# Kernel tuning notes

Measured on AMD Instinct MI355X. Metric: run time of the kernel, lower is better.

## Reference

```python
import jax, jax.numpy as jnp
import numpy as np

D = 16        # flow dimensionality (args.d)
M = 128       # hidden nodes per layer
L = 2         # num_hidden_layers
B = 256       # batch
NF = 2        # num_flows
NORM_C = 1.0  # get_normalizing_const for initialization='sqrt-(m)'
STD_H = 1.0 / np.sqrt(M)  # give_std('sqrt-(m)', M)
STD_A = 0.1   # std for last layer


def _lower_mask(out, inp, d):
    # block lower-triangular (incl. diagonal) mask over d x d blocks
    return jnp.kron(jnp.tril(jnp.ones((d, d), jnp.float32)), jnp.ones((out // d, inp // d), jnp.float32))


def _diag_blocks(W, d):
    # extract the d diagonal blocks of W -> (d, out_blk, in_blk)
    ob, ib = W.shape[0] // d, W.shape[1] // d
    idx = jnp.arange(d)
    return W.reshape(d, ob, d, ib)[idx, :, idx, :]


def _init_W(key, out, inp, d, std):
    # 'clamp-zero' init: positive diagonal blocks, gaussian strictly-lower blocks, zero above
    W = std * jax.random.normal(key, (out, inp), dtype=jnp.float32)
    lm = _lower_mask(out, inp, d)
    dm = jnp.kron(jnp.eye(d, dtype=jnp.float32), jnp.ones((out // d, inp // d), jnp.float32))
    W = W * lm
    return jnp.where(dm > 0, jnp.clip(jnp.abs(W), 1e-10, None), W)


def _flow(inp, Ws, bs, d, norm_c):
    b = inp.shape[0]
    out, grad = inp, None
    nlay = len(bs)
    log_c = jnp.log(jnp.asarray(norm_c, inp.dtype))
    for i in range(nlay):
        W = Ws[i]
        wm = W * _lower_mask(W.shape[0], W.shape[1], d)
        lg = jnp.log(_diag_blocks(W, d))            # (d, ob, ib)
        if grad is None:
            grad = jnp.broadcast_to(lg[None], (b,) + lg.shape)  # (B, d, ob, 1)
        else:
            # log-space matvec over previous width: (B,d,ob,1)
            grad = jax.nn.logsumexp(lg[None, :, :, :, None] + grad[:, :, None, :, :], axis=3)
        out = out @ wm.T + bs[i]                    # (B, ob*d)
        # log |tanh'(out)| = 2*(log2 - out - softplus(-2 out))
        lga = 2.0 * (jnp.log(2.0) - out - jax.nn.softplus(-2.0 * out))
        out = norm_c * jnp.tanh(out)
        ob = W.shape[0] // d
        grad = grad + lga.reshape(b, d, ob, 1) + log_c
    # final (linear) layer
    W = Ws[nlay]
    wm = W * _lower_mask(W.shape[0], W.shape[1], d)
    lg = jnp.log(_diag_blocks(W, d))                # (d, 1, ib)
    grad = jax.nn.logsumexp(lg[None, :, :, :, None] + grad[:, :, None, :, :], axis=3)  # (B,d,1,1)
    out = out @ wm.T                                # (B, d)
    return out, grad.reshape(b, d).sum(-1)          # log-det Jacobian per sample


def setup_inputs() -> dict:
    key = jax.random.key(0)
    ks = jax.random.split(key, 11)
    inp = jax.random.normal(ks[0], (B, D), dtype=jnp.float32)
    params = {}
    for f in range(NF):
        o = 1 + 5 * f
        params[f'f{f}_W0'] = _init_W(ks[o + 0], M * D, D, D, STD_H)
        params[f'f{f}_W1'] = _init_W(ks[o + 1], M * D, M * D, D, STD_H)
        params[f'f{f}_W2'] = _init_W(ks[o + 2], D, M * D, D, STD_A)
        params[f'f{f}_b0'] = STD_H * jax.random.normal(ks[o + 3], (M * D,), dtype=jnp.float32)
        params[f'f{f}_b1'] = STD_H * jax.random.normal(ks[o + 4], (M * D,), dtype=jnp.float32)
    return {'inp': inp, **params}


def reference(inp, f0_W0, f0_W1, f0_W2, f0_b0, f0_b1, f1_W0, f1_W1, f1_W2, f1_b0, f1_b1):
    out, ld0 = _flow(inp, [f0_W0, f0_W1, f0_W2], [f0_b0, f0_b1], D, NORM_C)
    out, ld1 = _flow(out, [f1_W0, f1_W1, f1_W2], [f1_b0, f1_b1], D, NORM_C)
    return out, ld0 + ld1
```

## Files before the change

### kernel.cpp

```cpp
#include <hip/hip_runtime.h>
#include <stdint.h>

#define BATCH 256
#define DBLK  16
#define OB    128
#define NN    2048

using bf16x8  = __attribute__((ext_vector_type(8))) __bf16;
using f32x4   = __attribute__((ext_vector_type(4))) float;
using ushort8 = __attribute__((ext_vector_type(8))) unsigned short;

__device__ __forceinline__ unsigned short f2bf(float f) {
    union { float f; uint32_t u; } v; v.f = f;
    uint32_t u = v.u;
    uint32_t r = (u + 0x7fffu + ((u >> 16) & 1u)) >> 16;
    return (unsigned short)r;
}

__device__ __forceinline__ float bf2f(unsigned short h) {
    union { uint32_t u; float f; } v; v.u = ((uint32_t)h) << 16;
    return v.f;
}

__device__ __forceinline__ void act_tanh_lga(float x, float& th, float& lga) {
    float ax = fabsf(x);
    float e  = __expf(-2.f * ax);
    float p  = 1.f + e;
    float t  = 1.f - __fdividef(2.f * e, p);
    th  = (x < 0.f) ? -t : t;
    lga = 2.f * (0.69314718055994531f - ax - __logf(p));
}

__device__ __forceinline__ ushort8 pack_bf8(float4 a, float4 b) {
    ushort8 u;
    u[0] = f2bf(a.x); u[1] = f2bf(a.y); u[2] = f2bf(a.z); u[3] = f2bf(a.w);
    u[4] = f2bf(b.x); u[5] = f2bf(b.y); u[6] = f2bf(b.z); u[7] = f2bf(b.w);
    return u;
}

__device__ __forceinline__ void conv4pairs(int cid, int tid,
                                           const float* __restrict__ Wsrc,
                                           unsigned short* __restrict__ Wdst) {
    float4 va[3][2];
    unsigned short* dp[3];
    bool act[3];
    #pragma unroll
    for (int i = 0; i < 3; ++i) {
        const int c = tid + i * 512;
        act[i] = (c < 1088);
        if (act[i]) {
            const int pi  = c / 272;
            const int rem = c - pi * 272;
            const int p   = cid * 4 + pi;
            const int kend0 = ((p >> 7) + 1) * OB;
            const int off = rem * 8;
            const int row = (off < kend0) ? p : (NN - 1 - p);
            const int k   = (off < kend0) ? off : (off - kend0);
            const float* sp = Wsrc + (size_t)row * NN + k;
            dp[i] = Wdst + (size_t)row * NN + k;
            va[i][0] = *(const float4*)(sp);
            va[i][1] = *(const float4*)(sp + 4);
        }
    }
    #pragma unroll
    for (int i = 0; i < 3; ++i)
        if (act[i]) *(ushort8*)dp[i] = pack_bf8(va[i][0], va[i][1]);
}

__device__ __forceinline__ void l0_block512(const float* __restrict__ xs,
                                            const float* __restrict__ W0,
                                            const float* __restrict__ b0,
                                            unsigned short* __restrict__ h0,
                                            unsigned short* __restrict__ e0,
                                            float* __restrict__ mmax,
                                            int b, int t) {
    const int dd = t >> 5;
    const int j0 = dd * OB + (t & 31) * 4;
    float g[4];
    unsigned short hv[4];
    float lm = -1e30f;
    #pragma unroll
    for (int q = 0; q < 4; ++q) {
        const int j = j0 + q;
        const float* wrow = W0 + (size_t)j * DBLK;
        float s = b0[j];
        #pragma unroll
        for (int c = 0; c < DBLK; c += 4) {
            float4 wv = *(const float4*)(wrow + c);
            s += wv.x * xs[c] + wv.y * xs[c + 1] + wv.z * xs[c + 2] + wv.w * xs[c + 3];
        }
        float th, lga;
        act_tanh_lga(s, th, lga);
        hv[q] = f2bf(th);
        g[q]  = __logf(wrow[dd]) + lga;
        lm = fmaxf(lm, g[q]);
    }
    #pragma unroll
    for (int off = 1; off < 32; off <<= 1) lm = fmaxf(lm, __shfl_xor(lm, off));
    ushort4 hh, ee;
    #pragma unroll
    for (int q = 0; q < 4; ++q) {
        ((unsigned short*)&hh)[q] = hv[q];
        ((unsigned short*)&ee)[q] = f2bf(__expf(g[q] - lm));
    }
    *(ushort4*)(h0 + (size_t)b * NN + j0) = hh;
    *(ushort4*)(e0 + (size_t)b * NN + j0) = ee;
    if ((t & 31) == 0) mmax[b * DBLK + dd] = lm;
}

__global__ void __launch_bounds__(512)
k_prep(const float* __restrict__ W1a,
       unsigned short* __restrict__ W1bf,
       const float* __restrict__ inp,
       const float* __restrict__ W00,
       const float* __restrict__ b00,
       unsigned short* __restrict__ h0,
       unsigned short* __restrict__ e0,
       float* __restrict__ mmax) {
    const int gb = blockIdx.x;
    const int t  = threadIdx.x;
    if (gb < 256) {
        conv4pairs(gb, t, W1a, W1bf);
    } else {
        const int b = gb - 256;
        l0_block512(inp + (size_t)b * DBLK, W00, b00, h0, e0, mmax, b, t);
    }
}

template<bool CONV>
__global__ void __launch_bounds__(512, 4)
k_l1(const unsigned short* __restrict__ h0,
     const unsigned short* __restrict__ W1b,
     const float* __restrict__ b1v,
     const unsigned short* __restrict__ e0,
     const float* __restrict__ mmax,
     unsigned short* __restrict__ h1,
     float* __restrict__ g1,
     const float* __restrict__ W1next,
     unsigned short* __restrict__ W1bfn) {
    const int tid = threadIdx.x;

    if (CONV && blockIdx.z == 4) {
        const int cid = (int)blockIdx.x * 16 + (int)blockIdx.y;
        conv4pairs(cid, tid, W1next, W1bfn);
        return;
    }

    const int dd    = blockIdx.x;
    const int bt    = blockIdx.y;
    const int ct    = blockIdx.z;
    const int w     = tid >> 6;
    const int lane  = tid & 63;
    const int brow0 = bt * 16;
    const int arow  = brow0 + (lane & 15);
    const int koff  = (lane >> 4) * 8;
    const int ncol  = lane & 15;
    const int col0  = dd * OB + ct * 32;

    f32x4 acc[2], acc2[2];
    #pragma unroll
    for (int nt = 0; nt < 2; ++nt) {
        acc[nt]  = (f32x4){0.f, 0.f, 0.f, 0.f};
        acc2[nt] = (f32x4){0.f, 0.f, 0.f, 0.f};
    }

    const unsigned short* Ab = h0 + (size_t)arow * NN + koff;
    const unsigned short* Bb[2];
    #pragma unroll
    for (int nt = 0; nt < 2; ++nt)
        Bb[nt] = W1b + (size_t)(col0 + nt * 16 + ncol) * NN + koff;

    bf16x8 ga  = {};
    bf16x8 gb0 = {};
    bf16x8 gb1 = {};
    if (w < 4) {
        const int k2 = dd * OB + w * 32;
        ga  = *(const bf16x8*)(e0 + (size_t)arow * NN + koff + k2);
        gb0 = *(const bf16x8*)(Bb[0] + k2);
        gb1 = *(const bf16x8*)(Bb[1] + k2);
    }

    const int nch = (dd + 1) * 4;
    #pragma unroll 4
    for (int c = w; c < nch; c += 8) {
        const int k = c * 32;
        bf16x8 a   = *(const bf16x8*)(Ab + k);
        bf16x8 b0v = *(const bf16x8*)(Bb[0] + k);
        bf16x8 b1w = *(const bf16x8*)(Bb[1] + k);
        acc[0] = __builtin_amdgcn_mfma_f32_16x16x32_bf16(a, b0v, acc[0], 0, 0, 0);
        acc[1] = __builtin_amdgcn_mfma_f32_16x16x32_bf16(a, b1w, acc[1], 0, 0, 0);
    }

    if (w < 4) {
        acc2[0] = __builtin_amdgcn_mfma_f32_16x16x32_bf16(ga, gb0, acc2[0], 0, 0, 0);
        acc2[1] = __builtin_amdgcn_mfma_f32_16x16x32_bf16(ga, gb1, acc2[1], 0, 0, 0);
    }

    __shared__ float ls1[8][2][64][4];
    __shared__ float ls2[4][2][64][4];
    #pragma unroll
    for (int nt = 0; nt < 2; ++nt)
        *(f32x4*)&ls1[w][nt][lane][0] = acc[nt];
    if (w < 4) {
        #pragma unroll
        for (int nt = 0; nt < 2; ++nt)
            *(f32x4*)&ls2[w][nt][lane][0] = acc2[nt];
    }
    __syncthreads();

    {
        const int o  = tid;
        const int rr = o >> 5;
        const int cc = o & 31;
        const int nt = cc >> 4;
        const int r  = rr & 3;
        const int ls = (rr >> 2) * 16 + (cc & 15);
        float S = 0.f, S2 = 0.f;
        #pragma unroll
        for (int ww = 0; ww < 8; ++ww) S += ls1[ww][nt][ls][r];
        #pragma unroll
        for (int ww = 0; ww < 4; ++ww) S2 += ls2[ww][nt][ls][r];
        const int j    = col0 + cc;
        const int brow = brow0 + rr;
        const float pre = S + b1v[j];
        float th, lga;
        act_tanh_lga(pre, th, lga);
        h1[(size_t)brow * NN + j] = f2bf(th);
        g1[(size_t)brow * NN + j] = __logf(S2) + mmax[brow * DBLK + dd] + lga;
    }
}

__device__ __forceinline__ float final_compute(const unsigned short* __restrict__ h1,
                                               const float* __restrict__ g1,
                                               const float* __restrict__ W2,
                                               int b, int t,
                                               float* sh, float* gf, float* sx) {
    const int wave = t >> 6;
    const int lane = t & 63;
    {
        const int k = t * 4;
        ushort4 hv = *(const ushort4*)(h1 + (size_t)b * NN + k);
        float4 f0;
        f0.x = bf2f(hv.x); f0.y = bf2f(hv.y); f0.z = bf2f(hv.z); f0.w = bf2f(hv.w);
        *(float4*)(sh + k) = f0;
    }
    __syncthreads();

    #pragma unroll
    for (int q = 0; q < 2; ++q) {
        const int dd = wave + q * 8;
        const float* w2r = W2 + (size_t)dd * NN;
        const int kend = (dd + 1) * OB;
        float s = 0.f;
        for (int k = lane * 4; k < kend; k += 64 * 4) {
            float4 hv = *(const float4*)(sh + k);
            float4 wv = *(const float4*)(w2r + k);
            s += hv.x * wv.x + hv.y * wv.y + hv.z * wv.z + hv.w * wv.w;
        }
        #pragma unroll
        for (int off = 32; off > 0; off >>= 1) s += __shfl_xor(s, off);
        float v0 = g1[(size_t)b * NN + dd * OB + lane];
        float v1 = g1[(size_t)b * NN + dd * OB + 64 + lane];
        float m = fmaxf(v0, v1);
        #pragma unroll
        for (int off = 32; off > 0; off >>= 1) m = fmaxf(m, __shfl_xor(m, off));
        float e = __expf(v0 - m) * w2r[dd * OB + lane]
                + __expf(v1 - m) * w2r[dd * OB + 64 + lane];
        #pragma unroll
        for (int off = 32; off > 0; off >>= 1) e += __shfl_xor(e, off);
        if (lane == 0) {
            sx[dd] = s;
            gf[dd] = __logf(e) + m;
        }
    }
    __syncthreads();
    float ld = 0.f;
    #pragma unroll
    for (int dd = 0; dd < DBLK; ++dd) ld += gf[dd];
    return ld;
}

__global__ void __launch_bounds__(512)
k_fin0(const unsigned short* __restrict__ h1,
       const float* __restrict__ g1,
       const float* __restrict__ W2,
       const float* __restrict__ W0n,
       const float* __restrict__ b0n,
       unsigned short* __restrict__ h0,
       unsigned short* __restrict__ e0,
       float* __restrict__ mmax,
       float* __restrict__ ld0) {
    __shared__ float sh[NN];
    __shared__ float gf[DBLK];
    __shared__ float sx[DBLK];
    const int b = blockIdx.x;
    const int t = threadIdx.x;
    float ld = final_compute(h1, g1, W2, b, t, sh, gf, sx);
    if (t == 0) ld0[b] = ld;
    l0_block512(sx, W0n, b0n, h0, e0, mmax, b, t);
}

__global__ void __launch_bounds__(512)
k_fin1(const unsigned short* __restrict__ h1,
       const float* __restrict__ g1,
       const float* __restrict__ W2,
       const float* __restrict__ ld0,
       float* __restrict__ out_final,
       float* __restrict__ ld_final) {
    __shared__ float sh[NN];
    __shared__ float gf[DBLK];
    __shared__ float sx[DBLK];
    const int b = blockIdx.x;
    const int t = threadIdx.x;
    float ld = final_compute(h1, g1, W2, b, t, sh, gf, sx);
    if (t < DBLK) out_final[b * DBLK + t] = sx[t];
    if (t == 0) ld_final[b] = ld + ld0[b];
}

extern "C" void kernel_launch(void* const* d_in, const int* in_sizes, int n_in,
                              void* d_out, int out_size, void* d_ws, size_t ws_size,
                              hipStream_t stream) {
    const float* inp   = (const float*)d_in[0];
    const float* W0[2] = {(const float*)d_in[1], (const float*)d_in[6]};
    const float* W1[2] = {(const float*)d_in[2], (const float*)d_in[7]};
    const float* W2[2] = {(const float*)d_in[3], (const float*)d_in[8]};
    const float* b0[2] = {(const float*)d_in[4], (const float*)d_in[9]};
    const float* b1[2] = {(const float*)d_in[5], (const float*)d_in[10]};

    char* w = (char*)d_ws;
    size_t off = 0;
    unsigned short* W1bf = (unsigned short*)(w + off); off += (size_t)2 * NN * NN * 2;
    unsigned short* h0b  = (unsigned short*)(w + off); off += (size_t)BATCH * NN * 2;
    unsigned short* e0b  = (unsigned short*)(w + off); off += (size_t)BATCH * NN * 2;
    float* mmax = (float*)(w + off); off += (size_t)BATCH * DBLK * 4;
    unsigned short* h1 = (unsigned short*)(w + off); off += (size_t)BATCH * NN * 2;
    float* g1   = (float*)(w + off); off += (size_t)BATCH * NN * 4;
    float* ld0  = (float*)(w + off); off += (size_t)BATCH * 4;

    float* out_final = (float*)d_out;
    float* ld_final  = (float*)d_out + BATCH * DBLK;

    k_prep<<<dim3(512), dim3(512), 0, stream>>>(
        W1[0], W1bf, inp, W0[0], b0[0], h0b, e0b, mmax);

    k_l1<true><<<dim3(DBLK, 16, 5), dim3(512), 0, stream>>>(
        h0b, W1bf, b1[0], e0b, mmax, h1, g1,
        W1[1], W1bf + (size_t)NN * NN);

    k_fin0<<<dim3(BATCH), dim3(512), 0, stream>>>(
        h1, g1, W2[0], W0[1], b0[1], h0b, e0b, mmax, ld0);

    k_l1<false><<<dim3(DBLK, 16, 4), dim3(512), 0, stream>>>(
        h0b, W1bf + (size_t)NN * NN, b1[1], e0b, mmax, h1, g1,
        nullptr, nullptr);

    k_fin1<<<dim3(BATCH), dim3(512), 0, stream>>>(
        h1, g1, W2[1], ld0, out_final, ld_final);
}
```

Baseline: 86.64 us.

## Widen layer-1 tiles to 32 batch rows and reschedule conversion blocks

```diff
diff --git a/kernel.cpp b/kernel.cpp
--- a/kernel.cpp
+++ b/kernel.cpp
@@ -38,20 +38,20 @@
     return u;
 }
 
-__device__ __forceinline__ void conv4pairs(int cid, int tid,
+__device__ __forceinline__ void conv8pairs(int cid, int tid,
                                            const float* __restrict__ Wsrc,
                                            unsigned short* __restrict__ Wdst) {
-    float4 va[3][2];
-    unsigned short* dp[3];
-    bool act[3];
-    #pragma unroll
-    for (int i = 0; i < 3; ++i) {
+    float4 va[5][2];
+    unsigned short* dp[5];
+    bool act[5];
+    #pragma unroll
+    for (int i = 0; i < 5; ++i) {
         const int c = tid + i * 512;
-        act[i] = (c < 1088);
+        act[i] = (c < 2176);
         if (act[i]) {
             const int pi  = c / 272;
             const int rem = c - pi * 272;
-            const int p   = cid * 4 + pi;
+            const int p   = cid * 8 + pi;
             const int kend0 = ((p >> 7) + 1) * OB;
             const int off = rem * 8;
             const int row = (off < kend0) ? p : (NN - 1 - p);
@@ -63,7 +63,7 @@
         }
     }
     #pragma unroll
-    for (int i = 0; i < 3; ++i)
+    for (int i = 0; i < 5; ++i)
         if (act[i]) *(ushort8*)dp[i] = pack_bf8(va[i][0], va[i][1]);
 }
 
@@ -119,16 +119,16 @@
        float* __restrict__ mmax) {
     const int gb = blockIdx.x;
     const int t  = threadIdx.x;
-    if (gb < 256) {
-        conv4pairs(gb, t, W1a, W1bf);
+    if (gb < 128) {
+        conv8pairs(gb, t, W1a, W1bf);
     } else {
-        const int b = gb - 256;
+        const int b = gb - 128;
         l0_block512(inp + (size_t)b * DBLK, W00, b00, h0, e0, mmax, b, t);
     }
 }
 
 template<bool CONV>
-__global__ void __launch_bounds__(512, 4)
+__global__ void __launch_bounds__(512, 2)
 k_l1(const unsigned short* __restrict__ h0,
      const unsigned short* __restrict__ W1b,
      const float* __restrict__ b1v,
@@ -140,88 +140,105 @@
      unsigned short* __restrict__ W1bfn) {
     const int tid = threadIdx.x;
 
-    if (CONV && blockIdx.z == 4) {
-        const int cid = (int)blockIdx.x * 16 + (int)blockIdx.y;
-        conv4pairs(cid, tid, W1next, W1bfn);
-        return;
-    }
-
-    const int dd    = blockIdx.x;
-    const int bt    = blockIdx.y;
+    int dd;
+    if (CONV) {
+        if (blockIdx.x < 4) {
+            const int cid = (int)blockIdx.x * 32 + (int)blockIdx.y * 4 + (int)blockIdx.z;
+            conv8pairs(cid, tid, W1next, W1bfn);
+            return;
+        }
+        dd = 19 - (int)blockIdx.x;
+    } else {
+        dd = 15 - (int)blockIdx.x;
+    }
+    const int btp   = blockIdx.y;
     const int ct    = blockIdx.z;
     const int w     = tid >> 6;
     const int lane  = tid & 63;
-    const int brow0 = bt * 16;
-    const int arow  = brow0 + (lane & 15);
+    const int brow0 = btp * 32;
+    const int arow0 = brow0 + (lane & 15);
+    const int arow1 = arow0 + 16;
     const int koff  = (lane >> 4) * 8;
     const int ncol  = lane & 15;
     const int col0  = dd * OB + ct * 32;
 
-    f32x4 acc[2], acc2[2];
-    #pragma unroll
-    for (int nt = 0; nt < 2; ++nt) {
-        acc[nt]  = (f32x4){0.f, 0.f, 0.f, 0.f};
-        acc2[nt] = (f32x4){0.f, 0.f, 0.f, 0.f};
-    }
-
-    const unsigned short* Ab = h0 + (size_t)arow * NN + koff;
+    f32x4 acc[2][2], acc2[2][2];
+    #pragma unroll
+    for (int hh = 0; hh < 2; ++hh)
+        #pragma unroll
+        for (int nt = 0; nt < 2; ++nt) {
+            acc[hh][nt]  = (f32x4){0.f, 0.f, 0.f, 0.f};
+            acc2[hh][nt] = (f32x4){0.f, 0.f, 0.f, 0.f};
+        }
+
+    const unsigned short* Ab0 = h0 + (size_t)arow0 * NN + koff;
+    const unsigned short* Ab1 = h0 + (size_t)arow1 * NN + koff;
     const unsigned short* Bb[2];
     #pragma unroll
     for (int nt = 0; nt < 2; ++nt)
         Bb[nt] = W1b + (size_t)(col0 + nt * 16 + ncol) * NN + koff;
 
-    bf16x8 ga  = {};
-    bf16x8 gb0 = {};
-    bf16x8 gb1 = {};
+    bf16x8 ga0 = {}, ga1 = {}, gb0 = {}, gb1 = {};
     if (w < 4) {
         const int k2 = dd * OB + w * 32;
-        ga  = *(const bf16x8*)(e0 + (size_t)arow * NN + koff + k2);
+        ga0 = *(const bf16x8*)(e0 + (size_t)arow0 * NN + koff + k2);
+        ga1 = *(const bf16x8*)(e0 + (size_t)arow1 * NN + koff + k2);
         gb0 = *(const bf16x8*)(Bb[0] + k2);
         gb1 = *(const bf16x8*)(Bb[1] + k2);
     }
 
     const int nch = (dd + 1) * 4;
-    #pragma unroll 4
+    #pragma unroll 2
     for (int c = w; c < nch; c += 8) {
         const int k = c * 32;
-        bf16x8 a   = *(const bf16x8*)(Ab + k);
+        bf16x8 a0  = *(const bf16x8*)(Ab0 + k);
+        bf16x8 a1  = *(const bf16x8*)(Ab1 + k);
         bf16x8 b0v = *(const bf16x8*)(Bb[0] + k);
         bf16x8 b1w = *(const bf16x8*)(Bb[1] + k);
-        acc[0] = __builtin_amdgcn_mfma_f32_16x16x32_bf16(a, b0v, acc[0], 0, 0, 0);
-        acc[1] = __builtin_amdgcn_mfma_f32_16x16x32_bf16(a, b1w, acc[1], 0, 0, 0);
+        acc[0][0] = __builtin_amdgcn_mfma_f32_16x16x32_bf16(a0, b0v, acc[0][0], 0, 0, 0);
+        acc[0][1] = __builtin_amdgcn_mfma_f32_16x16x32_bf16(a0, b1w, acc[0][1], 0, 0, 0);
+        acc[1][0] = __builtin_amdgcn_mfma_f32_16x16x32_bf16(a1, b0v, acc[1][0], 0, 0, 0);
+        acc[1][1] = __builtin_amdgcn_mfma_f32_16x16x32_bf16(a1, b1w, acc[1][1], 0, 0, 0);
     }
 
     if (w < 4) {
-        acc2[0] = __builtin_amdgcn_mfma_f32_16x16x32_bf16(ga, gb0, acc2[0], 0, 0, 0);
-        acc2[1] = __builtin_amdgcn_mfma_f32_16x16x32_bf16(ga, gb1, acc2[1], 0, 0, 0);
-    }
-
-    __shared__ float ls1[8][2][64][4];
-    __shared__ float ls2[4][2][64][4];
-    #pragma unroll
-    for (int nt = 0; nt < 2; ++nt)
-        *(f32x4*)&ls1[w][nt][lane][0] = acc[nt];
+        acc2[0][0] = __builtin_amdgcn_mfma_f32_16x16x32_bf16(ga0, gb0, acc2[0][0], 0, 0, 0);
+        acc2[0][1] = __builtin_amdgcn_mfma_f32_16x16x32_bf16(ga0, gb1, acc2[0][1], 0, 0, 0);
+        acc2[1][0] = __builtin_amdgcn_mfma_f32_16x16x32_bf16(ga1, gb0, acc2[1][0], 0, 0, 0);
+        acc2[1][1] = __builtin_amdgcn_mfma_f32_16x16x32_bf16(ga1, gb1, acc2[1][1], 0, 0, 0);
+    }
+
+    __shared__ float ls1[8][2][2][64][4];
+    __shared__ float ls2[4][2][2][64][4];
+    #pragma unroll
+    for (int hh = 0; hh < 2; ++hh)
+        #pragma unroll
+        for (int nt = 0; nt < 2; ++nt)
+            *(f32x4*)&ls1[w][hh][nt][lane][0] = acc[hh][nt];
     if (w < 4) {
         #pragma unroll
-        for (int nt = 0; nt < 2; ++nt)
-            *(f32x4*)&ls2[w][nt][lane][0] = acc2[nt];
+        for (int hh = 0; hh < 2; ++hh)
+            #pragma unroll
+            for (int nt = 0; nt < 2; ++nt)
+                *(f32x4*)&ls2[w][hh][nt][lane][0] = acc2[hh][nt];
     }
     __syncthreads();
 
-    {
-        const int o  = tid;
-        const int rr = o >> 5;
-        const int cc = o & 31;
-        const int nt = cc >> 4;
-        const int r  = rr & 3;
-        const int ls = (rr >> 2) * 16 + (cc & 15);
+    #pragma unroll
+    for (int half = 0; half < 2; ++half) {
+        const int o   = tid;
+        const int rr2 = o >> 5;
+        const int cc  = o & 31;
+        const int nt  = cc >> 4;
+        const int r   = rr2 & 3;
+        const int ls  = (rr2 >> 2) * 16 + (cc & 15);
         float S = 0.f, S2 = 0.f;
         #pragma unroll
-        for (int ww = 0; ww < 8; ++ww) S += ls1[ww][nt][ls][r];
-        #pragma unroll
-        for (int ww = 0; ww < 4; ++ww) S2 += ls2[ww][nt][ls][r];
+        for (int ww = 0; ww < 8; ++ww) S += ls1[ww][half][nt][ls][r];
+        #pragma unroll
+        for (int ww = 0; ww < 4; ++ww) S2 += ls2[ww][half][nt][ls][r];
         const int j    = col0 + cc;
-        const int brow = brow0 + rr;
+        const int brow = brow0 + half * 16 + rr2;
         const float pre = S + b1v[j];
         float th, lga;
         act_tanh_lga(pre, th, lga);
@@ -340,17 +357,17 @@
     float* out_final = (float*)d_out;
     float* ld_final  = (float*)d_out + BATCH * DBLK;
 
-    k_prep<<<dim3(512), dim3(512), 0, stream>>>(
+    k_prep<<<dim3(384), dim3(512), 0, stream>>>(
         W1[0], W1bf, inp, W0[0], b0[0], h0b, e0b, mmax);
 
-    k_l1<true><<<dim3(DBLK, 16, 5), dim3(512), 0, stream>>>(
+    k_l1<true><<<dim3(20, 8, 4), dim3(512), 0, stream>>>(
         h0b, W1bf, b1[0], e0b, mmax, h1, g1,
         W1[1], W1bf + (size_t)NN * NN);
 
     k_fin0<<<dim3(BATCH), dim3(512), 0, stream>>>(
         h1, g1, W2[0], W0[1], b0[1], h0b, e0b, mmax, ld0);
 
-    k_l1<false><<<dim3(DBLK, 16, 4), dim3(512), 0, stream>>>(
+    k_l1<false><<<dim3(16, 8, 4), dim3(512), 0, stream>>>(
         h0b, W1bf + (size_t)NN * NN, b1[1], e0b, mmax, h1, g1,
         nullptr, nullptr);
 
```

Result: faster. 76.75 us (-11.4%).
